# Optimization experiments

Measured on AMD Instinct MI355X. Metric: run time of the kernel, lower is better.

The kernel has to match this reference:

```python
import jax, jax.numpy as jnp
import numpy as np

D_IN, D_HIDDEN, DT_RANK, D_MEM, STEP = 256, 64, 16, 128, 16
B_, L_ = 2, 2048
S = 0.02  # weight init scale

def generate_a(d_in, d_hidden):
    i = jnp.arange(d_in, dtype=jnp.float32)[:, None]
    j = jnp.arange(d_hidden, dtype=jnp.float32)[None, :]
    off = jnp.sqrt(2.0 * i + 1.0) * jnp.sqrt(2.0 * j + 1.0)
    return jnp.where(i == j, i + 1.0, jnp.where(i > j, off, 0.0))

def setup_inputs():
    key = jax.random.key(0)
    ks = jax.random.split(key, 10)
    d_out = 3 * D_HIDDEN + 2 * D_IN + 2 * DT_RANK
    return {
        "x": jax.random.normal(ks[0], (B_, L_, D_IN), jnp.float32),
        "W_xproj": jax.random.normal(ks[1], (D_IN, d_out), jnp.float32) * S,
        "W_dt": jax.random.normal(ks[2], (DT_RANK, D_IN), jnp.float32) * S,
        "b_dt": jnp.full((D_IN,), -11.0, jnp.float32),
        "W_dtl": jax.random.normal(ks[3], (DT_RANK, D_IN), jnp.float32) * S,
        "b_dtl": jnp.full((D_IN,), -11.0, jnp.float32),
        "A": generate_a(D_IN, D_HIDDEN),
        "Dp": jnp.ones((D_IN,), jnp.float32),
        "W_Q": jax.random.normal(ks[4], (D_IN, D_MEM), jnp.float32) * S,
        "b_Q": jnp.zeros((D_MEM,), jnp.float32),
        "W_K": jax.random.normal(ks[5], (D_IN, D_MEM), jnp.float32) * S,
        "b_K": jnp.zeros((D_MEM,), jnp.float32),
        "W_V": jax.random.normal(ks[6], (D_IN, D_MEM), jnp.float32) * S,
        "b_V": jnp.zeros((D_MEM,), jnp.float32),
        "W_O": jax.random.normal(ks[7], (D_MEM, D_IN), jnp.float32) * S,
        "b_O": jnp.zeros((D_IN,), jnp.float32),
    }

def _selective_scan(u, delta, A, Bm, Cm, Dp):
    # u, delta: (b,l,d); A: (d,n); Bm, Cm: (b,l,n)
    dA = jnp.exp(jnp.einsum('bld,dn->bldn', delta, A))          # (b,l,d,n)
    dBu = delta[..., None] * Bm[:, :, None, :] * u[..., None]   # (b,l,d,n)
    def comb(e1, e2):
        a1, b1 = e1
        a2, b2 = e2
        return a2 * a1, a2 * b1 + b2
    _, xs = jax.lax.associative_scan(comb, (dA, dBu), axis=1)   # states (b,l,d,n)
    y = jnp.einsum('bldn,bln->bld', xs, Cm)
    if Dp is not None:
        y = y + u * Dp
    return y

def reference(x, W_xproj, W_dt, b_dt, W_dtl, b_dtl, A, Dp, W_Q, b_Q, W_K, b_K, W_V, b_V, W_O, b_O):
    proj = x @ W_xproj  # (b,l,3n+2d+2r)
    splits = np.cumsum([D_HIDDEN, D_HIDDEN, D_HIDDEN, D_IN, D_IN, DT_RANK]).tolist()
    Bm, Bl, Cm, E, Fg, dt, dtl = jnp.split(proj, splits, axis=-1)
    delta = jax.nn.softplus(dt @ W_dt + b_dt)       # delta_softplus=True folded in
    delta_l = jax.nn.softplus(dtl @ W_dtl + b_dtl)
    y = _selective_scan(x, delta, A, Bm, Cm, Dp)
    y_local = _selective_scan(x, delta_l, A, Bl, jnp.ones_like(Bl), None)  # C=ones, D=None
    memory = y_local[:, ::STEP, :]                  # strided checkpoints (b,m,d)
    Q = x @ W_Q + b_Q
    K = memory @ W_K + b_K
    V = memory @ W_V + b_V
    # note: original scales by sqrt(d_hidden), not sqrt(d_memory)
    w = jax.nn.softmax(jnp.einsum('blm,bkm->blk', Q, K) / jnp.sqrt(jnp.float32(D_HIDDEN)), axis=-1)
    att = jnp.einsum('blk,bkm->blm', w, V) @ W_O + b_O
    return y + att * E + x * Fg
```

## Files before the change

kernel.cpp:

```cpp
#include <hip/hip_runtime.h>
#include <math.h>

#define D_INN 256
#define D_HID 64
#define DTR 16
#define D_MEMM 128
#define BB 2
#define LL 2048
#define NROWS (BB*LL)
#define NPROJ 736
#define NTOT 864
#define SEG 16
#define SEGLEN (LL/SEG)

typedef __attribute__((ext_vector_type(8))) short short8v;
typedef __attribute__((ext_vector_type(4))) float float4v;

static __device__ __forceinline__ unsigned short f2bf(float f) {
    unsigned int u = __float_as_uint(f);
    u += 0x7fff + ((u >> 16) & 1);
    return (unsigned short)(u >> 16);
}

static __device__ __forceinline__ float rdlane(float v, int l) {
    return __uint_as_float(__builtin_amdgcn_readlane(__float_as_uint(v), l));
}

__global__ __launch_bounds__(256) void k_gemm(const float* __restrict__ x,
        const float* __restrict__ Wx, const float* __restrict__ Wq,
        const float* __restrict__ bq, float* __restrict__ proj) {
    __shared__ unsigned short As[64][40];
    __shared__ unsigned short Bs[64][40];
    const int t = threadIdx.x;
    const int lane = t & 63, w = t >> 6;
    const int wr = w >> 1, wc = w & 1;
    const int row0 = blockIdx.y * 64, col0 = blockIdx.x * 64;

    float4v acc[2][2];
    #pragma unroll
    for (int i = 0; i < 2; i++)
        #pragma unroll
        for (int j = 0; j < 2; j++) acc[i][j] = (float4v)0.f;

    const int ar = t >> 2, akq = (t & 3) * 8;
    const int bk = t >> 3, bcq = (t & 7) * 8;

    for (int k0 = 0; k0 < D_INN; k0 += 32) {
        float4 a0 = *(const float4*)&x[(size_t)(row0 + ar) * D_INN + k0 + akq];
        float4 a1 = *(const float4*)&x[(size_t)(row0 + ar) * D_INN + k0 + akq + 4];
        float4 b0 = {}, b1 = {};
        int col = col0 + bcq;
        if (col + 8 <= NPROJ) {
            b0 = *(const float4*)&Wx[(size_t)(k0 + bk) * NPROJ + col];
            b1 = *(const float4*)&Wx[(size_t)(k0 + bk) * NPROJ + col + 4];
        } else if (col < NTOT) {
            b0 = *(const float4*)&Wq[(size_t)(k0 + bk) * D_MEMM + (col - NPROJ)];
            b1 = *(const float4*)&Wq[(size_t)(k0 + bk) * D_MEMM + (col - NPROJ) + 4];
        }
        __syncthreads();
        {
            unsigned short av[8] = { f2bf(a0.x), f2bf(a0.y), f2bf(a0.z), f2bf(a0.w),
                                     f2bf(a1.x), f2bf(a1.y), f2bf(a1.z), f2bf(a1.w) };
            *(short8v*)&As[ar][akq] = *(short8v*)av;
            Bs[bcq + 0][bk] = f2bf(b0.x); Bs[bcq + 1][bk] = f2bf(b0.y);
            Bs[bcq + 2][bk] = f2bf(b0.z); Bs[bcq + 3][bk] = f2bf(b0.w);
            Bs[bcq + 4][bk] = f2bf(b1.x); Bs[bcq + 5][bk] = f2bf(b1.y);
            Bs[bcq + 6][bk] = f2bf(b1.z); Bs[bcq + 7][bk] = f2bf(b1.w);
        }
        __syncthreads();
        short8v af[2], bf[2];
        const int fr = lane & 15, fk = (lane >> 4) * 8;
        af[0] = *(short8v*)&As[wr * 32 + fr][fk];
        af[1] = *(short8v*)&As[wr * 32 + 16 + fr][fk];
        bf[0] = *(short8v*)&Bs[wc * 32 + fr][fk];
        bf[1] = *(short8v*)&Bs[wc * 32 + 16 + fr][fk];
        #pragma unroll
        for (int i = 0; i < 2; i++)
            #pragma unroll
            for (int j = 0; j < 2; j++)
                acc[i][j] = __builtin_amdgcn_mfma_f32_16x16x32_bf16(af[i], bf[j], acc[i][j], 0, 0, 0);
    }
    #pragma unroll
    for (int i = 0; i < 2; i++)
        #pragma unroll
        for (int j = 0; j < 2; j++)
            #pragma unroll
            for (int e = 0; e < 4; e++) {
                int rr = row0 + wr * 32 + i * 16 + (lane >> 4) * 4 + e;
                int cc = col0 + wc * 32 + j * 16 + (lane & 15);
                if (cc < NTOT) {
                    float v = acc[i][j][e];
                    if (cc >= NPROJ) v += bq[cc - NPROJ];
                    proj[(size_t)rr * NTOT + cc] = v;
                }
            }
}

__global__ __launch_bounds__(256) void k_xt(const float* __restrict__ x,
        float* __restrict__ xT) {
    __shared__ float tile[64][65];
    const int t = threadIdx.x;
    const int lt = blockIdx.x * 64, dt = blockIdx.y * 64, b = blockIdx.z;
    const int c = t & 63, rg = (t >> 6) * 16;
    #pragma unroll
    for (int j = 0; j < 16; ++j)
        tile[rg + j][c] = x[((size_t)b * LL + lt + rg + j) * D_INN + dt + c];
    __syncthreads();
    #pragma unroll
    for (int j = 0; j < 16; ++j)
        xT[((size_t)b * D_INN + dt + rg + j) * LL + lt + c] = tile[c][rg + j];
}

__global__ __launch_bounds__(256) void k_delta(const float* __restrict__ proj,
        const float* __restrict__ Wdt, const float* __restrict__ bdt,
        const float* __restrict__ Wdtl, const float* __restrict__ bdtl,
        float* __restrict__ deltaT, float* __restrict__ deltalT) {
    __shared__ float sdt[16][17], sdtl[16][17];
    const int t = threadIdx.x;
    const int r0 = blockIdx.x * 16;
    const int b = r0 >> 11, l0 = r0 & (LL - 1);
    {
        int r = t >> 4, c = t & 15;
        sdt[r][c]  = proj[(size_t)(r0 + r) * NTOT + 704 + c];
        sdtl[r][c] = proj[(size_t)(r0 + r) * NTOT + 720 + c];
    }
    __syncthreads();
    float w1[DTR], w2[DTR];
    #pragma unroll
    for (int r = 0; r < DTR; r++) {
        w1[r] = Wdt[r * D_INN + t];
        w2[r] = Wdtl[r * D_INN + t];
    }
    const float b1 = bdt[t], b2 = bdtl[t];
    float o1[16], o2[16];
    #pragma unroll
    for (int row = 0; row < 16; ++row) {
        float a1 = b1, a2 = b2;
        #pragma unroll
        for (int r = 0; r < DTR; r++) {
            a1 += sdt[row][r] * w1[r];
            a2 += sdtl[row][r] * w2[r];
        }
        o1[row] = (a1 > 20.f) ? a1 : log1pf(expf(a1));
        o2[row] = (a2 > 20.f) ? a2 : log1pf(expf(a2));
    }
    float* p1 = &deltaT[((size_t)b * D_INN + t) * LL + l0];
    float* p2 = &deltalT[((size_t)b * D_INN + t) * LL + l0];
    #pragma unroll
    for (int j = 0; j < 16; j += 4) {
        *(float4*)&p1[j] = make_float4(o1[j], o1[j+1], o1[j+2], o1[j+3]);
        *(float4*)&p2[j] = make_float4(o2[j], o2[j+1], o2[j+2], o2[j+3]);
    }
}

__global__ __launch_bounds__(256) void k_scan1(const float* __restrict__ xT,
        const float* __restrict__ proj, const float* __restrict__ A,
        const float* __restrict__ deltaT, const float* __restrict__ deltalT,
        float* __restrict__ Qbuf, float* __restrict__ SDbuf,
        float* __restrict__ cumd, float* __restrict__ mem) {
    const int t = threadIdx.x;
    const int w = t >> 6, n = t & 63;
    const int b = blockIdx.y;
    const int scan = blockIdx.z >> 4, seg = blockIdx.z & 15;
    const int d = blockIdx.x * 4 + w;
    const size_t rowbase = (size_t)b * LL + (size_t)seg * SEGLEN;
    const float* dT = (scan == 0 ? deltaT : deltalT) + ((size_t)b * D_INN + d) * LL + seg * SEGLEN;
    const float* uT = xT + ((size_t)b * D_INN + d) * LL + seg * SEGLEN;
    const int cB = (scan == 0) ? 0 : 64;
    const float Aln = A[d * D_HID + n] * 1.44269504f;
    const int lr = n & 7;

    float s = 0.f, sd = 0.f;
    for (int c = 0; c < SEGLEN / 8; ++c) {
        const size_t l0 = rowbase + c * 8;
        float dvl = dT[c * 8 + lr];
        float pl  = dvl * uT[c * 8 + lr];
        float Bv[8];
        #pragma unroll
        for (int li = 0; li < 8; ++li) Bv[li] = proj[(l0 + li) * NTOT + cB + n];
        #pragma unroll
        for (int li = 0; li < 8; ++li) {
            float dv = rdlane(dvl, li);
            float p  = rdlane(pl, li);
            s = fmaf(exp2f(dv * Aln), s, p * Bv[li]);
            sd += dv;
            if (scan == 1 && li == 0 && (c & 1) == 0) {
                float v = s;
                #pragma unroll
                for (int off = 32; off >= 1; off >>= 1) v += __shfl_xor(v, off);
                if (n == 0) {
                    int k = seg * 8 + (c >> 1);
                    mem[((size_t)b * 128 + k) * D_INN + d] = v;
                    cumd[(((size_t)b * SEG + seg) * 8 + (c >> 1)) * D_INN + d] = sd;
                }
            }
        }
    }
    Qbuf[((((size_t)scan * 2 + b) * SEG + seg) * D_INN + d) * 64 + n] = s;
    if (n == 0) SDbuf[(((size_t)scan * 2 + b) * SEG + seg) * D_INN + d] = sd;
}

__global__ __launch_bounds__(256) void k_scan2(const float* __restrict__ xT,
        const float* __restrict__ proj, const float* __restrict__ A,
        const float* __restrict__ Dp, const float* __restrict__ deltaT,
        const float* __restrict__ Qbuf, const float* __restrict__ SDbuf,
        float* __restrict__ y) {
    __shared__ float rbuf[4][8][65];
    const int t = threadIdx.x;
    const int w = t >> 6, n = t & 63;
    const int b = blockIdx.y, seg = blockIdx.z;
    const int d = blockIdx.x * 4 + w;
    const size_t rowbase = (size_t)b * LL + (size_t)seg * SEGLEN;
    const float* dT = deltaT + ((size_t)b * D_INN + d) * LL + seg * SEGLEN;
    const float* uT = xT + ((size_t)b * D_INN + d) * LL + seg * SEGLEN;
    const float Aln = A[d * D_HID + n] * 1.44269504f;
    const float Dpv = Dp[d];
    const int lr = n & 7;
    const int rli = n >> 3, g = n & 7;

    float s = 0.f;
    for (int k = 0; k < seg; ++k) {
        float sdk = SDbuf[(((size_t)b * SEG + k) * D_INN + d)];
        float Qk = Qbuf[(((size_t)b * SEG + k) * D_INN + d) * 64 + n];
        s = fmaf(exp2f(sdk * Aln), s, Qk);
    }

    for (int c = 0; c < SEGLEN / 8; ++c) {
        const size_t l0 = rowbase + c * 8;
        float dvl = dT[c * 8 + lr];
        float uvl = uT[c * 8 + lr];
        float pl = dvl * uvl;
        float Bv[8], Cv[8];
        #pragma unroll
        for (int li = 0; li < 8; ++li) {
            Bv[li] = proj[(l0 + li) * NTOT + n];
            Cv[li] = proj[(l0 + li) * NTOT + 128 + n];
        }
        #pragma unroll
        for (int li = 0; li < 8; ++li) {
            float dv = rdlane(dvl, li);
            float p  = rdlane(pl, li);
            s = fmaf(exp2f(dv * Aln), s, p * Bv[li]);
            rbuf[w][li][n] = s * Cv[li];
        }
        float acc = 0.f;
        #pragma unroll
        for (int j = 0; j < 8; ++j) acc += rbuf[w][rli][g * 8 + j];
        acc += __shfl_xor(acc, 1);
        acc += __shfl_xor(acc, 2);
        acc += __shfl_xor(acc, 4);
        float uv = __shfl(uvl, rli);
        if (g == 0) {
            y[(l0 + rli) * D_INN + d] = acc + uv * Dpv;
        }
    }
}

__global__ __launch_bounds__(256) void k_sin(const float* __restrict__ A,
        const float* __restrict__ Qbuf, const float* __restrict__ SDbuf,
        float* __restrict__ Sin) {
    const int t = threadIdx.x, w = t >> 6, n = t & 63;
    const int b = blockIdx.y;
    const int d = blockIdx.x * 4 + w;
    const float Aln = A[d * D_HID + n] * 1.44269504f;
    float s = 0.f;
    #pragma unroll
    for (int seg = 0; seg < SEG; ++seg) {
        if (seg > 0) Sin[(((size_t)b * SEG + seg) * D_INN + d) * 64 + n] = s;
        float sdk = SDbuf[((size_t)(2 + b) * SEG + seg) * D_INN + d];
        float Qk = Qbuf[(((size_t)(2 + b) * SEG + seg) * D_INN + d) * 64 + n];
        s = fmaf(exp2f(sdk * Aln), s, Qk);
    }
}

__global__ __launch_bounds__(256) void k_fix(const float* __restrict__ A,
        const float* __restrict__ Sin, const float* __restrict__ cumd,
        float* __restrict__ mem) {
    const int t = threadIdx.x, w = t >> 6, n = t & 63;
    const int k = 8 + blockIdx.y;
    const int b = blockIdx.z;
    const int d = blockIdx.x * 4 + w;
    const int seg = k >> 3;
    const float Aln = A[d * D_HID + n] * 1.44269504f;
    float cum = cumd[((size_t)b * 128 + k) * D_INN + d];
    float sv = Sin[(((size_t)b * SEG + seg) * D_INN + d) * 64 + n];
    float v = exp2f(cum * Aln) * sv;
    #pragma unroll
    for (int off = 32; off >= 1; off >>= 1) v += __shfl_xor(v, off);
    if (n == 0) mem[((size_t)b * 128 + k) * D_INN + d] += v;
}

__global__ __launch_bounds__(128) void k_kvwo(const float* __restrict__ mem,
        const float* __restrict__ Wk, const float* __restrict__ bk,
        const float* __restrict__ Wv, const float* __restrict__ bv,
        const float* __restrict__ Wo,
        float* __restrict__ K, float* __restrict__ VWo) {
    __shared__ float mrow[256];
    __shared__ float vrow[128];
    const int k = blockIdx.x, b = blockIdx.y;
    const int t = threadIdx.x;
    const float* mr = mem + ((size_t)b * 128 + k) * D_INN;
    mrow[t] = mr[t];
    mrow[t + 128] = mr[t + 128];
    __syncthreads();
    float aK = bk[t], aV = bv[t];
    for (int dd = 0; dd < D_INN; dd++) {
        float m = mrow[dd];
        aK += m * Wk[dd * D_MEMM + t];
        aV += m * Wv[dd * D_MEMM + t];
    }
    K[((size_t)b * 128 + k) * D_MEMM + t] = aK;
    vrow[t] = aV;
    __syncthreads();
    float a0 = 0.f, a1 = 0.f;
    for (int m = 0; m < 128; ++m) {
        float vm = vrow[m];
        a0 += vm * Wo[(size_t)m * D_INN + t];
        a1 += vm * Wo[(size_t)m * D_INN + t + 128];
    }
    VWo[((size_t)b * 128 + k) * D_INN + t] = a0;
    VWo[((size_t)b * 128 + k) * D_INN + t + 128] = a1;
}

__global__ __launch_bounds__(256) void k_attn(const float* __restrict__ x,
        const float* __restrict__ proj, const float* __restrict__ y,
        const float* __restrict__ K, const float* __restrict__ VWo,
        const float* __restrict__ bo, float* __restrict__ out) {
    __shared__ float qs[16][132];
    __shared__ float ws[16][132];
    __shared__ float denom[16];
    const int t = threadIdx.x;
    const int b = blockIdx.y;
    const int r0 = blockIdx.x * 16;
    const size_t rowbase = (size_t)b * LL + r0;
    {
        int r = t >> 4, c8 = (t & 15) * 8;
        const float* src = &proj[(rowbase + r) * NTOT + NPROJ + c8];
        *(float4*)&qs[r][c8] = *(const float4*)src;
        *(float4*)&qs[r][c8 + 4] = *(const float4*)(src + 4);
    }
    __syncthreads();
    {
        const int k = t & 127, rg = (t >> 7) * 8;
        const float* Kr = K + ((size_t)b * 128 + k) * D_MEMM;
        float acc[8] = {};
        #pragma unroll 8
        for (int m = 0; m < 128; m += 4) {
            float4 kv = *(const float4*)&Kr[m];
            #pragma unroll
            for (int r = 0; r < 8; ++r) {
                float4 qv = *(const float4*)&qs[rg + r][m];
                acc[r] += qv.x * kv.x + qv.y * kv.y + qv.z * kv.z + qv.w * kv.w;
            }
        }
        #pragma unroll
        for (int r = 0; r < 8; ++r) ws[rg + r][k] = acc[r] * 0.125f;
    }
    __syncthreads();
    {
        const int r = t >> 4, j = t & 15;
        float4 v0 = *(float4*)&ws[r][j * 8];
        float4 v1 = *(float4*)&ws[r][j * 8 + 4];
        float mx = fmaxf(fmaxf(fmaxf(v0.x, v0.y), fmaxf(v0.z, v0.w)),
                         fmaxf(fmaxf(v1.x, v1.y), fmaxf(v1.z, v1.w)));
        #pragma unroll
        for (int o = 1; o < 16; o <<= 1) mx = fmaxf(mx, __shfl_xor(mx, o));
        v0.x = expf(v0.x - mx); v0.y = expf(v0.y - mx);
        v0.z = expf(v0.z - mx); v0.w = expf(v0.w - mx);
        v1.x = expf(v1.x - mx); v1.y = expf(v1.y - mx);
        v1.z = expf(v1.z - mx); v1.w = expf(v1.w - mx);
        float sum = v0.x + v0.y + v0.z + v0.w + v1.x + v1.y + v1.z + v1.w;
        #pragma unroll
        for (int o = 1; o < 16; o <<= 1) sum += __shfl_xor(sum, o);
        *(float4*)&ws[r][j * 8] = v0;
        *(float4*)&ws[r][j * 8 + 4] = v1;
        if (j == 0) denom[r] = sum;
    }
    __syncthreads();
    {
        const int w = t >> 6, lane = t & 63;
        const int c0 = lane * 4;
        const float* vb = VWo + (size_t)b * 128 * D_INN + c0;
        float acc[4][4] = {};
        #pragma unroll 8
        for (int k = 0; k < 128; k += 4) {
            float4 wv[4];
            #pragma unroll
            for (int r = 0; r < 4; ++r) wv[r] = *(float4*)&ws[w * 4 + r][k];
            #pragma unroll
            for (int kk = 0; kk < 4; ++kk) {
                float4 vw = *(const float4*)&vb[(size_t)(k + kk) * D_INN];
                #pragma unroll
                for (int r = 0; r < 4; ++r) {
                    float wk = (kk == 0 ? wv[r].x : kk == 1 ? wv[r].y : kk == 2 ? wv[r].z : wv[r].w);
                    acc[r][0] += wk * vw.x; acc[r][1] += wk * vw.y;
                    acc[r][2] += wk * vw.z; acc[r][3] += wk * vw.w;
                }
            }
        }
        float4 bov = *(const float4*)&bo[c0];
        #pragma unroll
        for (int r = 0; r < 4; ++r) {
            size_t rr = rowbase + w * 4 + r;
            float dn = 1.f / denom[w * 4 + r];
            float4 yv = *(const float4*)&y[rr * D_INN + c0];
            float4 xv = *(const float4*)&x[rr * D_INN + c0];
            float4 Ev = *(const float4*)&proj[rr * NTOT + 192 + c0];
            float4 Fv = *(const float4*)&proj[rr * NTOT + 448 + c0];
            float4 o;
            o.x = yv.x + (acc[r][0] * dn + bov.x) * Ev.x + xv.x * Fv.x;
            o.y = yv.y + (acc[r][1] * dn + bov.y) * Ev.y + xv.y * Fv.y;
            o.z = yv.z + (acc[r][2] * dn + bov.z) * Ev.z + xv.z * Fv.z;
            o.w = yv.w + (acc[r][3] * dn + bov.w) * Ev.w + xv.w * Fv.w;
            *(float4*)&out[rr * D_INN + c0] = o;
        }
    }
}

extern "C" void kernel_launch(void* const* d_in, const int* in_sizes, int n_in,
                              void* d_out, int out_size, void* d_ws, size_t ws_size,
                              hipStream_t stream) {
    const float* x    = (const float*)d_in[0];
    const float* Wx   = (const float*)d_in[1];
    const float* Wdt  = (const float*)d_in[2];
    const float* bdt  = (const float*)d_in[3];
    const float* Wdtl = (const float*)d_in[4];
    const float* bdtl = (const float*)d_in[5];
    const float* A    = (const float*)d_in[6];
    const float* Dp   = (const float*)d_in[7];
    const float* Wq   = (const float*)d_in[8];
    const float* bq   = (const float*)d_in[9];
    const float* Wk   = (const float*)d_in[10];
    const float* bk   = (const float*)d_in[11];
    const float* Wv   = (const float*)d_in[12];
    const float* bv   = (const float*)d_in[13];
    const float* Wo   = (const float*)d_in[14];
    const float* bo   = (const float*)d_in[15];
    float* out = (float*)d_out;
    float* ws = (float*)d_ws;

    float* proj    = ws;
    float* deltaT  = proj + (size_t)NROWS * NTOT;
    float* deltalT = deltaT + (size_t)NROWS * D_INN;
    float* yb      = deltalT + (size_t)NROWS * D_INN;
    float* mem     = yb + (size_t)NROWS * D_INN;
    float* Kb      = mem + (size_t)BB * 128 * D_INN;
    float* Qbuf    = Kb + (size_t)BB * 128 * D_MEMM;
    float* SDbuf   = Qbuf + (size_t)4 * SEG * D_INN * 64;
    float* cumd    = SDbuf + (size_t)4 * SEG * D_INN;
    float* Sin     = cumd + (size_t)BB * SEG * 8 * D_INN;
    float* VWo     = Sin + (size_t)BB * SEG * D_INN * 64;
    float* xT      = VWo + (size_t)BB * 128 * D_INN;

    hipLaunchKernelGGL(k_gemm, dim3(14, 64), dim3(256), 0, stream, x, Wx, Wq, bq, proj);
    hipLaunchKernelGGL(k_xt, dim3(32, 4, 2), dim3(256), 0, stream, x, xT);
    hipLaunchKernelGGL(k_delta, dim3(NROWS / 16), dim3(256), 0, stream,
                       proj, Wdt, bdt, Wdtl, bdtl, deltaT, deltalT);
    hipLaunchKernelGGL(k_scan1, dim3(64, 2, 32), dim3(256), 0, stream,
                       xT, proj, A, deltaT, deltalT, Qbuf, SDbuf, cumd, mem);
    hipLaunchKernelGGL(k_scan2, dim3(64, 2, 16), dim3(256), 0, stream,
                       xT, proj, A, Dp, deltaT, Qbuf, SDbuf, yb);
    hipLaunchKernelGGL(k_sin, dim3(64, 2), dim3(256), 0, stream,
                       A, Qbuf, SDbuf, Sin);
    hipLaunchKernelGGL(k_fix, dim3(64, 120, 2), dim3(256), 0, stream,
                       A, Sin, cumd, mem);
    hipLaunchKernelGGL(k_kvwo, dim3(128, 2), dim3(128), 0, stream,
                       mem, Wk, bk, Wv, bv, Wo, Kb, VWo);
    hipLaunchKernelGGL(k_attn, dim3(128, 2), dim3(256), 0, stream,
                       x, proj, yb, Kb, VWo, bo, out);
}
```

Measured before the change: 222.7 us.

## Pack B/Bl/C projections into chunked layout for vectorized scan loads

The GEMM epilogue now writes the first 192 projection columns (B, Bl, C) into a packed layout indexed by chunk of 8 timesteps, state index and timestep, so the scan kernels can fetch the 8 values per lane with two float4 loads. Previously each lane read 8 scattered scalars from rows strided by 864 floats. The first scan kernel is also split into two template instantiations so the scan selection becomes compile-time and the checkpoint branch is hoisted out of the inner loop. Costs are an extra workspace buffer and a less coalesced GEMM store pattern for those columns.

```diff
diff --git a/kernel.cpp b/kernel.cpp
--- a/kernel.cpp
+++ b/kernel.cpp
@@ -12,6 +12,7 @@
 #define NTOT 864
 #define SEG 16
 #define SEGLEN (LL/SEG)
+#define NCHUNK (LL/8)
 
 typedef __attribute__((ext_vector_type(8))) short short8v;
 typedef __attribute__((ext_vector_type(4))) float float4v;
@@ -26,9 +27,12 @@
     return __uint_as_float(__builtin_amdgcn_readlane(__float_as_uint(v), l));
 }
 
+#define PK(g, b, chunk, n, li) (((((size_t)(g)*BB + (b)) * NCHUNK + (chunk)) * 64 + (n)) * 8 + (li))
+
 __global__ __launch_bounds__(256) void k_gemm(const float* __restrict__ x,
         const float* __restrict__ Wx, const float* __restrict__ Wq,
-        const float* __restrict__ bq, float* __restrict__ proj) {
+        const float* __restrict__ bq, float* __restrict__ proj,
+        float* __restrict__ packed) {
     __shared__ unsigned short As[64][40];
     __shared__ unsigned short Bs[64][40];
     const int t = threadIdx.x;
@@ -83,17 +87,23 @@
     #pragma unroll
     for (int i = 0; i < 2; i++)
         #pragma unroll
-        for (int j = 0; j < 2; j++)
-            #pragma unroll
-            for (int e = 0; e < 4; e++) {
-                int rr = row0 + wr * 32 + i * 16 + (lane >> 4) * 4 + e;
-                int cc = col0 + wc * 32 + j * 16 + (lane & 15);
-                if (cc < NTOT) {
+        for (int j = 0; j < 2; j++) {
+            int cc = col0 + wc * 32 + j * 16 + (lane & 15);
+            int rr0 = row0 + wr * 32 + i * 16 + (lane >> 4) * 4;
+            if (cc < 192) {
+                int g = cc >> 6, n = cc & 63;
+                int bb = rr0 >> 11, l = rr0 & (LL - 1);
+                float4 pk = make_float4(acc[i][j][0], acc[i][j][1], acc[i][j][2], acc[i][j][3]);
+                *(float4*)&packed[PK(g, bb, l >> 3, n, l & 7)] = pk;
+            } else {
+                #pragma unroll
+                for (int e = 0; e < 4; e++) {
                     float v = acc[i][j][e];
                     if (cc >= NPROJ) v += bq[cc - NPROJ];
-                    proj[(size_t)rr * NTOT + cc] = v;
+                    proj[(size_t)(rr0 + e) * NTOT + cc] = v;
                 }
             }
+        }
 }
 
 __global__ __launch_bounds__(256) void k_xt(const float* __restrict__ x,
@@ -153,55 +163,57 @@
     }
 }
 
-__global__ __launch_bounds__(256) void k_scan1(const float* __restrict__ xT,
-        const float* __restrict__ proj, const float* __restrict__ A,
-        const float* __restrict__ deltaT, const float* __restrict__ deltalT,
+template<int SCAN>
+__global__ __launch_bounds__(256) void k_scan1t(const float* __restrict__ xT,
+        const float* __restrict__ packed, const float* __restrict__ A,
+        const float* __restrict__ dTall,
         float* __restrict__ Qbuf, float* __restrict__ SDbuf,
         float* __restrict__ cumd, float* __restrict__ mem) {
     const int t = threadIdx.x;
     const int w = t >> 6, n = t & 63;
-    const int b = blockIdx.y;
-    const int scan = blockIdx.z >> 4, seg = blockIdx.z & 15;
+    const int b = blockIdx.y, seg = blockIdx.z;
     const int d = blockIdx.x * 4 + w;
-    const size_t rowbase = (size_t)b * LL + (size_t)seg * SEGLEN;
-    const float* dT = (scan == 0 ? deltaT : deltalT) + ((size_t)b * D_INN + d) * LL + seg * SEGLEN;
+    const float* dT = dTall + ((size_t)b * D_INN + d) * LL + seg * SEGLEN;
     const float* uT = xT + ((size_t)b * D_INN + d) * LL + seg * SEGLEN;
-    const int cB = (scan == 0) ? 0 : 64;
     const float Aln = A[d * D_HID + n] * 1.44269504f;
     const int lr = n & 7;
+    const float* Bp = packed + PK(SCAN, b, seg * 16, 0, 0);
 
     float s = 0.f, sd = 0.f;
-    for (int c = 0; c < SEGLEN / 8; ++c) {
-        const size_t l0 = rowbase + c * 8;
+    for (int c = 0; c < 16; ++c) {
         float dvl = dT[c * 8 + lr];
         float pl  = dvl * uT[c * 8 + lr];
-        float Bv[8];
-        #pragma unroll
-        for (int li = 0; li < 8; ++li) Bv[li] = proj[(l0 + li) * NTOT + cB + n];
-        #pragma unroll
-        for (int li = 0; li < 8; ++li) {
-            float dv = rdlane(dvl, li);
-            float p  = rdlane(pl, li);
+        float4 B0 = *(const float4*)&Bp[((size_t)c * 64 + n) * 8];
+        float4 B1 = *(const float4*)&Bp[((size_t)c * 64 + n) * 8 + 4];
+        float Bv[8] = {B0.x, B0.y, B0.z, B0.w, B1.x, B1.y, B1.z, B1.w};
+        {
+            float dv = rdlane(dvl, 0), p = rdlane(pl, 0);
+            s = fmaf(exp2f(dv * Aln), s, p * Bv[0]);
+            sd += dv;
+        }
+        if (SCAN == 1 && (c & 1) == 0) {
+            float v = s;
+            #pragma unroll
+            for (int off = 32; off >= 1; off >>= 1) v += __shfl_xor(v, off);
+            if (n == 0) {
+                int k = seg * 8 + (c >> 1);
+                mem[((size_t)b * 128 + k) * D_INN + d] = v;
+                cumd[(((size_t)b * SEG + seg) * 8 + (c >> 1)) * D_INN + d] = sd;
+            }
+        }
+        #pragma unroll
+        for (int li = 1; li < 8; ++li) {
+            float dv = rdlane(dvl, li), p = rdlane(pl, li);
             s = fmaf(exp2f(dv * Aln), s, p * Bv[li]);
             sd += dv;
-            if (scan == 1 && li == 0 && (c & 1) == 0) {
-                float v = s;
-                #pragma unroll
-                for (int off = 32; off >= 1; off >>= 1) v += __shfl_xor(v, off);
-                if (n == 0) {
-                    int k = seg * 8 + (c >> 1);
-                    mem[((size_t)b * 128 + k) * D_INN + d] = v;
-                    cumd[(((size_t)b * SEG + seg) * 8 + (c >> 1)) * D_INN + d] = sd;
-                }
-            }
-        }
-    }
-    Qbuf[((((size_t)scan * 2 + b) * SEG + seg) * D_INN + d) * 64 + n] = s;
-    if (n == 0) SDbuf[(((size_t)scan * 2 + b) * SEG + seg) * D_INN + d] = sd;
+        }
+    }
+    Qbuf[((((size_t)SCAN * 2 + b) * SEG + seg) * D_INN + d) * 64 + n] = s;
+    if (n == 0) SDbuf[(((size_t)SCAN * 2 + b) * SEG + seg) * D_INN + d] = sd;
 }
 
 __global__ __launch_bounds__(256) void k_scan2(const float* __restrict__ xT,
-        const float* __restrict__ proj, const float* __restrict__ A,
+        const float* __restrict__ packed, const float* __restrict__ A,
         const float* __restrict__ Dp, const float* __restrict__ deltaT,
         const float* __restrict__ Qbuf, const float* __restrict__ SDbuf,
         float* __restrict__ y) {
@@ -217,6 +229,8 @@
     const float Dpv = Dp[d];
     const int lr = n & 7;
     const int rli = n >> 3, g = n & 7;
+    const float* Bp = packed + PK(0, b, seg * 16, 0, 0);
+    const float* Cp = packed + PK(2, b, seg * 16, 0, 0);
 
     float s = 0.f;
     for (int k = 0; k < seg; ++k) {
@@ -225,17 +239,17 @@
         s = fmaf(exp2f(sdk * Aln), s, Qk);
     }
 
-    for (int c = 0; c < SEGLEN / 8; ++c) {
+    for (int c = 0; c < 16; ++c) {
         const size_t l0 = rowbase + c * 8;
         float dvl = dT[c * 8 + lr];
         float uvl = uT[c * 8 + lr];
         float pl = dvl * uvl;
-        float Bv[8], Cv[8];
-        #pragma unroll
-        for (int li = 0; li < 8; ++li) {
-            Bv[li] = proj[(l0 + li) * NTOT + n];
-            Cv[li] = proj[(l0 + li) * NTOT + 128 + n];
-        }
+        float4 B0 = *(const float4*)&Bp[((size_t)c * 64 + n) * 8];
+        float4 B1 = *(const float4*)&Bp[((size_t)c * 64 + n) * 8 + 4];
+        float4 C0 = *(const float4*)&Cp[((size_t)c * 64 + n) * 8];
+        float4 C1 = *(const float4*)&Cp[((size_t)c * 64 + n) * 8 + 4];
+        float Bv[8] = {B0.x, B0.y, B0.z, B0.w, B1.x, B1.y, B1.z, B1.w};
+        float Cv[8] = {C0.x, C0.y, C0.z, C0.w, C1.x, C1.y, C1.z, C1.w};
         #pragma unroll
         for (int li = 0; li < 8; ++li) {
             float dv = rdlane(dvl, li);
@@ -451,15 +465,18 @@
     float* Sin     = cumd + (size_t)BB * SEG * 8 * D_INN;
     float* VWo     = Sin + (size_t)BB * SEG * D_INN * 64;
     float* xT      = VWo + (size_t)BB * 128 * D_INN;
-
-    hipLaunchKernelGGL(k_gemm, dim3(14, 64), dim3(256), 0, stream, x, Wx, Wq, bq, proj);
+    float* packed  = xT + (size_t)NROWS * D_INN;
+
+    hipLaunchKernelGGL(k_gemm, dim3(14, 64), dim3(256), 0, stream, x, Wx, Wq, bq, proj, packed);
     hipLaunchKernelGGL(k_xt, dim3(32, 4, 2), dim3(256), 0, stream, x, xT);
     hipLaunchKernelGGL(k_delta, dim3(NROWS / 16), dim3(256), 0, stream,
                        proj, Wdt, bdt, Wdtl, bdtl, deltaT, deltalT);
-    hipLaunchKernelGGL(k_scan1, dim3(64, 2, 32), dim3(256), 0, stream,
-                       xT, proj, A, deltaT, deltalT, Qbuf, SDbuf, cumd, mem);
+    hipLaunchKernelGGL(k_scan1t<0>, dim3(64, 2, 16), dim3(256), 0, stream,
+                       xT, packed, A, deltaT, Qbuf, SDbuf, cumd, mem);
+    hipLaunchKernelGGL(k_scan1t<1>, dim3(64, 2, 16), dim3(256), 0, stream,
+                       xT, packed, A, deltalT, Qbuf, SDbuf, cumd, mem);
     hipLaunchKernelGGL(k_scan2, dim3(64, 2, 16), dim3(256), 0, stream,
-                       xT, proj, A, Dp, deltaT, Qbuf, SDbuf, yb);
+                       xT, packed, A, Dp, deltaT, Qbuf, SDbuf, yb);
     hipLaunchKernelGGL(k_sin, dim3(64, 2), dim3(256), 0, stream,
                        A, Qbuf, SDbuf, Sin);
     hipLaunchKernelGGL(k_fix, dim3(64, 120, 2), dim3(256), 0, stream,
```

Result: no change. 223.0 us (+0.2%).
